# Performance work log

Hardware: AMD Instinct MI355X
Metric: run time of the kernel (lower is better)

The kernel has to match this reference:

```python
import jax, jax.numpy as jnp
import numpy as np

N_NODES = 100000
N_EDGES = 500000
NUM_RADIAL = 6
HIDDEN = 128
SQRT3 = 1.7320508075688772


def swish(x):
    return x * jax.nn.sigmoid(x)


def setup_inputs() -> dict:
    key = jax.random.key(0)
    k1, k2, k3, k4, k5, k6 = jax.random.split(key, 6)
    x = jax.random.randint(k1, (N_NODES,), 0, 95)
    rbf = jax.random.normal(k2, (N_EDGES, NUM_RADIAL), dtype=jnp.float32)
    i = jax.random.randint(k3, (N_EDGES,), 0, N_NODES)
    j = jax.random.randint(k4, (N_EDGES,), 0, N_NODES)
    emb_weight = jax.random.uniform(k5, (95, HIDDEN), dtype=jnp.float32,
                                    minval=-SQRT3, maxval=SQRT3)
    w_rbf = jax.random.normal(k6, (NUM_RADIAL, HIDDEN), dtype=jnp.float32) / np.sqrt(NUM_RADIAL)
    b_rbf = jnp.zeros((HIDDEN,), dtype=jnp.float32)
    w_lin = jax.random.normal(jax.random.fold_in(key, 7), (3 * HIDDEN, HIDDEN),
                              dtype=jnp.float32) / np.sqrt(3 * HIDDEN)
    b_lin = jnp.zeros((HIDDEN,), dtype=jnp.float32)
    return {"x": x, "rbf": rbf, "i": i, "j": j, "emb_weight": emb_weight,
            "w_rbf": w_rbf, "b_rbf": b_rbf, "w_lin": w_lin, "b_lin": b_lin}


def reference(x, rbf, i, j, emb_weight, w_rbf, b_rbf, w_lin, b_lin):
    # node embeddings: [N, H]
    h = emb_weight[x]
    # rbf projection + swish: [E, H]
    r = swish(rbf @ w_rbf + b_rbf)
    # gather edge endpoints, concat -> [E, 3H], linear + swish -> [E, H]
    cat = jnp.concatenate([h[i], h[j], r], axis=-1)
    return swish(cat @ w_lin + b_lin)
```

## Files before the change

### kernel.cpp

```cpp
#include <hip/hip_runtime.h>
#include <hip/hip_bf16.h>

typedef short bf16x8 __attribute__((ext_vector_type(8)));
typedef float f32x4 __attribute__((ext_vector_type(4)));

#define HID 128
#define NRAD 6
#define TILE 64
#define SWS 132

static __device__ __forceinline__ unsigned short f2bf(float f) {
    union { float f; unsigned u; } v; v.f = f;
    unsigned r = v.u + 0x7FFFu + ((v.u >> 16) & 1u);
    return (unsigned short)(r >> 16);
}

static __device__ __forceinline__ unsigned cvt_pk_bf16(float lo, float hi) {
    unsigned r;
    asm("v_cvt_pk_bf16_f32 %0, %1, %2" : "=v"(r) : "v"(lo), "v"(hi));
    return r;
}

static __device__ __forceinline__ float swishf(float z) {
    return z * __builtin_amdgcn_rcpf(1.0f + __expf(-z));
}

__global__ void precompute_kernel(const float* __restrict__ emb,
                                  const float* __restrict__ w_lin,
                                  const float* __restrict__ b_lin,
                                  float* __restrict__ P1,
                                  float* __restrict__ P2,
                                  unsigned short* __restrict__ Wt) {
    const int b = blockIdx.x;
    const int t = threadIdx.x;
    if (b < 190) {
        const int v = (b < 95) ? b : b - 95;
        const float* W = w_lin + (b < 95 ? 0 : HID * HID);
        float acc = (b < 95) ? b_lin[t] : 0.0f;
        #pragma unroll 4
        for (int k = 0; k < HID; ++k)
            acc = fmaf(emb[v * HID + k], W[k * HID + t], acc);
        (b < 95 ? P1 : P2)[v * HID + t] = acc;
    } else {
        const int kr = b - 190;
        Wt[t * HID + kr] = f2bf(w_lin[(2 * HID + kr) * HID + t]);
    }
}

__global__ __launch_bounds__(256, 1) void edge_kernel(
    const float* __restrict__ rbf, const int* __restrict__ ei,
    const int* __restrict__ ej, const int* __restrict__ x,
    const float* __restrict__ w_rbf, const float* __restrict__ b_rbf,
    const float* __restrict__ P1, const float* __restrict__ P2,
    const unsigned short* __restrict__ Wt,
    float* __restrict__ out, int E, int ntiles)
{
    __shared__ __align__(16) float s_w[7 * SWS];
    __shared__ __align__(16) unsigned short sB[HID * HID];
    __shared__ __align__(16) float sOut[4 * 16 * 64];

    const int t = threadIdx.x;
    const int w = t >> 6, l = t & 63, lr = l & 15, lg = l >> 4;
    const int cidx = lr;
    const int eg   = lg;

    for (int idx = t; idx < 7 * HID; idx += 256) {
        const int q = idx >> 7, c = idx & 127;
        s_w[q * SWS + c] = (q < 6) ? w_rbf[idx] : b_rbf[c];
    }
    {
        const uint4* g = (const uint4*)Wt;
        #pragma unroll
        for (int q = 0; q < 8; ++q) {
            int gi = q * 256 + t;
            int n = gi >> 4, cc = gi & 15;
            uint4 v = g[gi];
            *(uint4*)((char*)sB + n * 256 + ((cc * 16) ^ ((n & 7) << 4))) = v;
        }
    }
    __syncthreads();

    char* const myOut = (char*)(sOut + w * 16 * 64);
    char* const myR   = myOut;

    int tile = blockIdx.x;

    float2 cr01[4], cr23[4], cr45[4];
    int xi, xj;
    {
        const int b0 = tile * TILE + w * 16;
        #pragma unroll
        for (int i = 0; i < 4; ++i) {
            const int ce = min(b0 + eg * 4 + i, E - 1);
            const float* rp = rbf + (size_t)ce * NRAD;
            cr01[i] = *(const float2*)rp;
            cr23[i] = *(const float2*)(rp + 2);
            cr45[i] = *(const float2*)(rp + 4);
        }
        const int e0 = min(b0 + lr, E - 1);
        xi = x[ei[e0]];
        xj = x[ej[e0]];
    }

    for (; tile < ntiles; tile += gridDim.x) {
        const int base = tile * TILE + w * 16;

        const float* p1 = P1 + xi * HID;
        const float* p2 = P2 + xj * HID;
        f32x4 a1[4], a2[4];
        #pragma unroll
        for (int fi = 0; fi < 4; ++fi) {
            const int n0 = fi * 16 + lg * 4;
            a1[fi] = *(const f32x4*)(p1 + n0);
            a2[fi] = *(const f32x4*)(p2 + n0);
        }

        const int tn = tile + gridDim.x;
        const int tnb = (tn < ntiles ? tn : tile) * TILE + w * 16;
        const int en = min(tnb + lr, E - 1);
        const int ni = ei[en];
        const int nj = ej[en];

        const float* bw = s_w + 6 * SWS + cidx * 8;
        const f32x4 bz0 = *(const f32x4*)bw;
        const f32x4 bz1 = *(const f32x4*)(bw + 4);
        f32x4 z0[4], z1[4];
        #pragma unroll
        for (int i = 0; i < 4; ++i) { z0[i] = bz0; z1[i] = bz1; }
        #pragma unroll
        for (int q = 0; q < NRAD; ++q) {
            const f32x4 w0 = *(const f32x4*)(s_w + q * SWS + cidx * 8);
            const f32x4 w1 = *(const f32x4*)(s_w + q * SWS + cidx * 8 + 4);
            #pragma unroll
            for (int i = 0; i < 4; ++i) {
                const float rq = (q == 0) ? cr01[i].x : (q == 1) ? cr01[i].y
                               : (q == 2) ? cr23[i].x : (q == 3) ? cr23[i].y
                               : (q == 4) ? cr45[i].x : cr45[i].y;
                #pragma unroll
                for (int u = 0; u < 4; ++u) {
                    z0[i][u] = fmaf(rq, w0[u], z0[i][u]);
                    z1[i][u] = fmaf(rq, w1[u], z1[i][u]);
                }
            }
        }
        #pragma unroll
        for (int i = 0; i < 4; ++i) {
            uint4 pk;
            pk.x = cvt_pk_bf16(swishf(z0[i][0]), swishf(z0[i][1]));
            pk.y = cvt_pk_bf16(swishf(z0[i][2]), swishf(z0[i][3]));
            pk.z = cvt_pk_bf16(swishf(z1[i][0]), swishf(z1[i][1]));
            pk.w = cvt_pk_bf16(swishf(z1[i][2]), swishf(z1[i][3]));
            const int row = eg * 4 + i;
            *(uint4*)(myR + row * 256 + ((cidx * 16) ^ ((row & 7) << 4))) = pk;
        }
        bf16x8 af[4];
        #pragma unroll
        for (int kk = 0; kk < 4; ++kk)
            af[kk] = *(const bf16x8*)(myR + lr * 256 +
                        ((kk * 64 + lg * 16) ^ ((lr & 7) << 4)));

        f32x4 b1[4], b2[4];
        #pragma unroll
        for (int fi = 0; fi < 4; ++fi) {
            const int n0 = 64 + fi * 16 + lg * 4;
            b1[fi] = *(const f32x4*)(p1 + n0);
            b2[fi] = *(const f32x4*)(p2 + n0);
        }

        float2 nr01[4], nr23[4], nr45[4];
        #pragma unroll
        for (int i = 0; i < 4; ++i) {
            const int ne = min(tnb + eg * 4 + i, E - 1);
            const float* rp = rbf + (size_t)ne * NRAD;
            nr01[i] = *(const float2*)rp;
            nr23[i] = *(const float2*)(rp + 2);
            nr45[i] = *(const float2*)(rp + 4);
        }
        const int nxi = x[ni];
        const int nxj = x[nj];

        #pragma unroll
        for (int h = 0; h < 2; ++h) {
            #pragma unroll
            for (int fi = 0; fi < 4; ++fi) {
                const int f = h * 4 + fi;
                f32x4 acc = (f32x4){0.f, 0.f, 0.f, 0.f};
                const int rowB = f * 16 + lr;
                const int rB = rowB * 256, sw2 = (rowB & 7) << 4;
                #pragma unroll
                for (int kk = 0; kk < 4; ++kk) {
                    const int colb = kk * 64 + lg * 16;
                    bf16x8 bb = *(const bf16x8*)((const char*)sB + rB + (colb ^ sw2));
                    acc = __builtin_amdgcn_mfma_f32_16x16x32_bf16(bb, af[kk], acc, 0, 0, 0);
                }
                const f32x4 g1 = h ? b1[fi] : a1[fi];
                const f32x4 g2 = h ? b2[fi] : a2[fi];
                const int n0h = (fi * 16 + lg * 4);
                f32x4 v;
                #pragma unroll
                for (int u = 0; u < 4; ++u)
                    v[u] = swishf(acc[u] + g1[u] + g2[u]);
                *(f32x4*)(myOut + lr * 256 + ((n0h * 4) ^ ((lr & 7) << 4))) = v;
            }

            #pragma unroll
            for (int it = 0; it < 4; ++it) {
                const int idx = it * 64 + l;
                const int row = idx >> 4, cc = idx & 15;
                const f32x4 v = *(const f32x4*)(myOut + row * 256 +
                                  ((cc * 16) ^ ((row & 7) << 4)));
                if (base + row < E)
                    __builtin_nontemporal_store(v,
                        (f32x4*)(out + (size_t)(base + row) * HID + h * 64 + cc * 4));
            }
        }

        #pragma unroll
        for (int i = 0; i < 4; ++i) {
            cr01[i] = nr01[i]; cr23[i] = nr23[i]; cr45[i] = nr45[i];
        }
        xi = nxi; xj = nxj;
    }
}

extern "C" void kernel_launch(void* const* d_in, const int* in_sizes, int n_in,
                              void* d_out, int out_size, void* d_ws, size_t ws_size,
                              hipStream_t stream) {
    const int*   x     = (const int*)  d_in[0];
    const float* rbf   = (const float*)d_in[1];
    const int*   ei    = (const int*)  d_in[2];
    const int*   ej    = (const int*)  d_in[3];
    const float* emb   = (const float*)d_in[4];
    const float* w_rbf = (const float*)d_in[5];
    const float* b_rbf = (const float*)d_in[6];
    const float* w_lin = (const float*)d_in[7];
    const float* b_lin = (const float*)d_in[8];
    float* out = (float*)d_out;
    const int E = in_sizes[2];

    float* P1 = (float*)d_ws;
    float* P2 = (float*)((char*)d_ws + 49152);
    unsigned short* Wt = (unsigned short*)((char*)d_ws + 98304);

    hipLaunchKernelGGL(precompute_kernel, dim3(318), dim3(128), 0, stream,
                       emb, w_lin, b_lin, P1, P2, Wt);

    const int ntiles = (E + TILE - 1) / TILE;
    const int nblk = ntiles < 768 ? ntiles : 768;
    hipLaunchKernelGGL(edge_kernel, dim3(nblk), dim3(256), 0, stream,
                       rbf, ei, ej, x, w_rbf, b_rbf, P1, P2, Wt, out, E, ntiles);
}
```

Before: 95.40 us.

## Compute rbf projection with a bf16 MFMA instead of scalar FMAs

Replaces the per-lane scalar FMA loop for rbf@w_rbf+b_rbf with a single 16x16x32 bf16 MFMA per output fragment. The weights and bias are packed once into register fragments, and the bias is folded in through a constant-one column. Each lane now loads one edge's rbf row instead of four, and the shared-memory weight table goes away. In exchange, the rbf inputs and weights are rounded to bf16 before the projection, which lowers precision. The MFMA also pads the K dimension from 7 to 32 with zeros.

```diff
diff --git a/kernel.cpp b/kernel.cpp
--- a/kernel.cpp
+++ b/kernel.cpp
@@ -7,7 +7,6 @@
 #define HID 128
 #define NRAD 6
 #define TILE 64
-#define SWS 132
 
 static __device__ __forceinline__ unsigned short f2bf(float f) {
     union { float f; unsigned u; } v; v.f = f;
@@ -55,19 +54,12 @@
     const unsigned short* __restrict__ Wt,
     float* __restrict__ out, int E, int ntiles)
 {
-    __shared__ __align__(16) float s_w[7 * SWS];
     __shared__ __align__(16) unsigned short sB[HID * HID];
     __shared__ __align__(16) float sOut[4 * 16 * 64];
 
     const int t = threadIdx.x;
     const int w = t >> 6, l = t & 63, lr = l & 15, lg = l >> 4;
-    const int cidx = lr;
-    const int eg   = lg;
-
-    for (int idx = t; idx < 7 * HID; idx += 256) {
-        const int q = idx >> 7, c = idx & 127;
-        s_w[q * SWS + c] = (q < 6) ? w_rbf[idx] : b_rbf[c];
-    }
+
     {
         const uint4* g = (const uint4*)Wt;
         #pragma unroll
@@ -78,6 +70,20 @@
             *(uint4*)((char*)sB + n * 256 + ((cc * 16) ^ ((n & 7) << 4))) = v;
         }
     }
+    bf16x8 wf6[8];
+    #pragma unroll
+    for (int f = 0; f < 8; ++f) {
+        union { unsigned short s[8]; bf16x8 v; } u8;
+        const int n = f * 16 + lr;
+        #pragma unroll
+        for (int u = 0; u < 8; ++u) {
+            float val = 0.f;
+            if (lg == 0) val = (u < NRAD) ? w_rbf[u * HID + n]
+                               : (u == 6 ? b_rbf[n] : 0.f);
+            u8.s[u] = f2bf(val);
+        }
+        wf6[f] = u8.v;
+    }
     __syncthreads();
 
     char* const myOut = (char*)(sOut + w * 16 * 64);
@@ -85,19 +91,15 @@
 
     int tile = blockIdx.x;
 
-    float2 cr01[4], cr23[4], cr45[4];
+    float2 r01, r23, r45;
     int xi, xj;
     {
         const int b0 = tile * TILE + w * 16;
-        #pragma unroll
-        for (int i = 0; i < 4; ++i) {
-            const int ce = min(b0 + eg * 4 + i, E - 1);
-            const float* rp = rbf + (size_t)ce * NRAD;
-            cr01[i] = *(const float2*)rp;
-            cr23[i] = *(const float2*)(rp + 2);
-            cr45[i] = *(const float2*)(rp + 4);
-        }
         const int e0 = min(b0 + lr, E - 1);
+        const float* rp = rbf + (size_t)e0 * NRAD;
+        r01 = *(const float2*)rp;
+        r23 = *(const float2*)(rp + 2);
+        r45 = *(const float2*)(rp + 4);
         xi = x[ei[e0]];
         xj = x[ej[e0]];
     }
@@ -121,37 +123,24 @@
         const int ni = ei[en];
         const int nj = ej[en];
 
-        const float* bw = s_w + 6 * SWS + cidx * 8;
-        const f32x4 bz0 = *(const f32x4*)bw;
-        const f32x4 bz1 = *(const f32x4*)(bw + 4);
-        f32x4 z0[4], z1[4];
-        #pragma unroll
-        for (int i = 0; i < 4; ++i) { z0[i] = bz0; z1[i] = bz1; }
-        #pragma unroll
-        for (int q = 0; q < NRAD; ++q) {
-            const f32x4 w0 = *(const f32x4*)(s_w + q * SWS + cidx * 8);
-            const f32x4 w1 = *(const f32x4*)(s_w + q * SWS + cidx * 8 + 4);
-            #pragma unroll
-            for (int i = 0; i < 4; ++i) {
-                const float rq = (q == 0) ? cr01[i].x : (q == 1) ? cr01[i].y
-                               : (q == 2) ? cr23[i].x : (q == 3) ? cr23[i].y
-                               : (q == 4) ? cr45[i].x : cr45[i].y;
-                #pragma unroll
-                for (int u = 0; u < 4; ++u) {
-                    z0[i][u] = fmaf(rq, w0[u], z0[i][u]);
-                    z1[i][u] = fmaf(rq, w1[u], z1[i][u]);
-                }
-            }
-        }
-        #pragma unroll
-        for (int i = 0; i < 4; ++i) {
-            uint4 pk;
-            pk.x = cvt_pk_bf16(swishf(z0[i][0]), swishf(z0[i][1]));
-            pk.y = cvt_pk_bf16(swishf(z0[i][2]), swishf(z0[i][3]));
-            pk.z = cvt_pk_bf16(swishf(z1[i][0]), swishf(z1[i][1]));
-            pk.w = cvt_pk_bf16(swishf(z1[i][2]), swishf(z1[i][3]));
-            const int row = eg * 4 + i;
-            *(uint4*)(myR + row * 256 + ((cidx * 16) ^ ((row & 7) << 4))) = pk;
+        union { unsigned u[4]; bf16x8 v; } rf;
+        rf.u[0] = (lg == 0) ? cvt_pk_bf16(r01.x, r01.y) : 0u;
+        rf.u[1] = (lg == 0) ? cvt_pk_bf16(r23.x, r23.y) : 0u;
+        rf.u[2] = (lg == 0) ? cvt_pk_bf16(r45.x, r45.y) : 0u;
+        rf.u[3] = (lg == 0) ? 0x00003F80u : 0u;
+
+        f32x4 dacc[8];
+        #pragma unroll
+        for (int f = 0; f < 8; ++f)
+            dacc[f] = __builtin_amdgcn_mfma_f32_16x16x32_bf16(
+                          wf6[f], rf.v, (f32x4){0.f, 0.f, 0.f, 0.f}, 0, 0, 0);
+
+        #pragma unroll
+        for (int f = 0; f < 8; ++f) {
+            unsigned q0 = cvt_pk_bf16(swishf(dacc[f][0]), swishf(dacc[f][1]));
+            unsigned q1 = cvt_pk_bf16(swishf(dacc[f][2]), swishf(dacc[f][3]));
+            uint2 pk = {q0, q1};
+            *(uint2*)(myR + lr * 256 + ((f * 32 + lg * 8) ^ ((lr & 7) << 4))) = pk;
         }
         bf16x8 af[4];
         #pragma unroll
@@ -167,14 +156,12 @@
             b2[fi] = *(const f32x4*)(p2 + n0);
         }
 
-        float2 nr01[4], nr23[4], nr45[4];
-        #pragma unroll
-        for (int i = 0; i < 4; ++i) {
-            const int ne = min(tnb + eg * 4 + i, E - 1);
-            const float* rp = rbf + (size_t)ne * NRAD;
-            nr01[i] = *(const float2*)rp;
-            nr23[i] = *(const float2*)(rp + 2);
-            nr45[i] = *(const float2*)(rp + 4);
+        float2 q01, q23, q45;
+        {
+            const float* rp = rbf + (size_t)en * NRAD;
+            q01 = *(const float2*)rp;
+            q23 = *(const float2*)(rp + 2);
+            q45 = *(const float2*)(rp + 4);
         }
         const int nxi = x[ni];
         const int nxj = x[nj];
@@ -215,10 +202,7 @@
             }
         }
 
-        #pragma unroll
-        for (int i = 0; i < 4; ++i) {
-            cr01[i] = nr01[i]; cr23[i] = nr23[i]; cr45[i] = nr45[i];
-        }
+        r01 = q01; r23 = q23; r45 = q45;
         xi = nxi; xj = nxj;
     }
 }
```

After: 94.36 us. About the same (-1.1%).
